# Kernel optimization log

Measured on AMD Instinct MI355X. Metric: run time of the kernel, lower is better.

The kernel has to match this reference:

```python
import jax, jax.numpy as jnp
import numpy as np

D_MODEL = 64


def _wn_weight(v, g):
    # weight_norm on Conv2d with default dim=0: per-output-channel normalization.
    # v: [O, I] (1x1 kernel squeezed), g: [O]
    norm = jnp.sqrt(jnp.sum(v * v, axis=1, keepdims=True))  # [O,1]
    return (g[:, None] / norm) * v  # [O, I]


def _conv1x1(x, v, g, b):
    # x: [B, I, L, V] -> [B, O, L, V]
    w = _wn_weight(v, g)
    return jnp.einsum('oi,bilv->bolv', w, x) + b[None, :, None, None]


def setup_inputs() -> dict:
    key = jax.random.key(0)
    ks = jax.random.split(key, 13)
    B, D, L, V = 2, D_MODEL, 4096, 4
    inp = {'queries': jax.random.normal(ks[0], (B, D, L, V), dtype=jnp.float32)}
    names = ['q', 'k', 'v', 'o']
    for i, n in enumerate(names):
        inp[n + '_v'] = jax.random.normal(ks[1 + 3 * i], (D, D), dtype=jnp.float32) * (1.0 / np.sqrt(D))
        inp[n + '_g'] = jnp.ones((D,), dtype=jnp.float32)
        inp[n + '_b'] = jnp.zeros((D,), dtype=jnp.float32)
    return inp


def reference(queries, q_v, q_g, q_b, k_v, k_g, k_b, v_v, v_g, v_b, o_v, o_g, o_b):
    B, D, L, V = queries.shape
    # 1x1 weight-normed conv projections, then permute(0,2,3,1) -> [B, L, V, D]
    q = jnp.transpose(_conv1x1(queries, q_v, q_g, q_b), (0, 2, 3, 1))
    k = jnp.transpose(_conv1x1(queries, k_v, k_g, k_b), (0, 2, 3, 1))
    v = jnp.transpose(_conv1x1(queries, v_v, v_g, v_b), (0, 2, 3, 1))
    scale = 1.0 / np.sqrt(D).astype(np.float32)
    # scores: [B, V(heads), L, S]
    scores = jnp.einsum('blhe,bshe->bhls', q, k)
    A = jax.nn.softmax(scale * scores, axis=-1)  # dropout p=0 -> identity
    out = jnp.einsum('bhls,bshd->blhd', A, v)  # [B, L, V, D]
    out = jnp.transpose(out, (0, 3, 1, 2))  # [B, D, L, V]
    out = _conv1x1(out, o_v, o_g, o_b)
    return queries + out
```

## Files before the change

### kernel.cpp

```cpp
#include <hip/hip_runtime.h>
#include <math.h>

#define D 64
#define L 4096
#define H 4
#define B 2
#define NBH 8
#define SPLIT 4
#define KTILES (L/64/SPLIT)
#define QSCALE 0.18033688011112042f

typedef unsigned short ushort_t;
typedef __attribute__((ext_vector_type(8)))  __bf16 bf16x8;
typedef __attribute__((ext_vector_type(2)))  __bf16 bf16x2;
typedef __attribute__((ext_vector_type(16))) float  f32x16;

union U4 { unsigned u[4]; bf16x8 v; };

#if __has_builtin(__builtin_amdgcn_exp2f)
__device__ __forceinline__ float EXP2(float x){ return __builtin_amdgcn_exp2f(x); }
#else
__device__ __forceinline__ float EXP2(float x){
    float r; asm("v_exp_f32 %0, %1" : "=v"(r) : "v"(x)); return r;
}
#endif

__device__ __forceinline__ unsigned pk(float lo, float hi){
    bf16x2 t; t.x = (__bf16)lo; t.y = (__bf16)hi;
    return __builtin_bit_cast(unsigned, t);
}
__device__ __forceinline__ ushort_t f2bf(float x){
    __bf16 h = (__bf16)x; return __builtin_bit_cast(ushort_t, h);
}
__device__ __forceinline__ float bf2f(ushort_t u){
    unsigned x = ((unsigned)u) << 16; return __builtin_bit_cast(float, x);
}

__device__ __forceinline__ void gload16(const void* g, void* l){
    __builtin_amdgcn_global_load_lds(
        (const __attribute__((address_space(1))) unsigned*)g,
        (__attribute__((address_space(3))) unsigned*)l, 16, 0, 0);
}

__device__ __forceinline__ bf16x8 ldfrag(const ushort_t* buf, int row, int cb){
    return *(const bf16x8*)(buf + row*64 + ((cb ^ (row&7)) << 3));
}

__global__ void wn_kernel(const float* __restrict__ qv, const float* __restrict__ qg,
                          const float* __restrict__ kv, const float* __restrict__ kg,
                          const float* __restrict__ vv, const float* __restrict__ vg,
                          const float* __restrict__ ov, const float* __restrict__ og,
                          float* __restrict__ W)
{
    int m = blockIdx.x;
    const float* v = (m==0)?qv:(m==1)?kv:(m==2)?vv:ov;
    const float* g = (m==0)?qg:(m==1)?kg:(m==2)?vg:og;
    int o = threadIdx.x;
    float ss = 0.f;
    #pragma unroll 8
    for (int i=0;i<D;i++){ float x = v[o*D+i]; ss += x*x; }
    float sc = g[o] / sqrtf(ss);
    #pragma unroll 8
    for (int i=0;i<D;i++) W[m*D*D + o*D + i] = sc * v[o*D+i];
}

__global__ __launch_bounds__(256) void proj_qkv_kernel(
    const float* __restrict__ X, const float* __restrict__ W,
    const float* __restrict__ qb, const float* __restrict__ kb, const float* __restrict__ vb,
    unsigned* __restrict__ Qd, unsigned* __restrict__ Kd, unsigned* __restrict__ Vtd)
{
    int chunk = blockIdx.x, b = blockIdx.y, m = blockIdx.z;
    const float* bias = (m==0)?qb:(m==1)?kb:vb;
    const float* Wm = W + m*(D*D);

    __shared__ __align__(16) float Xs[64][68];
    __shared__ __align__(16) float Wb[64][68];
    __shared__ __align__(16) float Os[64][68];

    int t = threadIdx.x;
    int p0 = chunk*64;
    const float* Xb = X + (size_t)b*D*(L*H);
    for (int idx=t; idx<1024; idx+=256){
        int o = idx>>4, i4 = idx&15;
        *(float4*)&Wb[o][i4*4] = *(const float4*)&Wm[o*64 + i4*4];
    }
    for (int idx=t; idx<1024; idx+=256){
        int i = idx>>4, p4 = idx&15;
        *(float4*)&Xs[i][p4*4] = *(const float4*)&Xb[(size_t)i*(L*H) + p0 + p4*4];
    }
    __syncthreads();

    int pg = t&15, og = t>>4;
    float acc[4][4];
    #pragma unroll
    for (int pp=0;pp<4;pp++)
        #pragma unroll
        for (int oo=0;oo<4;oo++) acc[pp][oo]=0.f;

    #pragma unroll 4
    for (int i4=0;i4<16;i4++){
        float4 xr[4], wr[4];
        #pragma unroll
        for (int di=0;di<4;di++) xr[di] = *(const float4*)&Xs[i4*4+di][pg*4];
        #pragma unroll
        for (int oo=0;oo<4;oo++) wr[oo] = *(const float4*)&Wb[og*4+oo][i4*4];
        #pragma unroll
        for (int pp=0;pp<4;pp++){
            #pragma unroll
            for (int oo=0;oo<4;oo++){
                acc[pp][oo] += ((const float*)&xr[0])[pp]*wr[oo].x
                             + ((const float*)&xr[1])[pp]*wr[oo].y
                             + ((const float*)&xr[2])[pp]*wr[oo].z
                             + ((const float*)&xr[3])[pp]*wr[oo].w;
            }
        }
    }
    float b4[4];
    #pragma unroll
    for (int oo=0;oo<4;oo++) b4[oo] = bias[og*4+oo];
    #pragma unroll
    for (int pp=0;pp<4;pp++){
        float4 o4 = make_float4(acc[pp][0]+b4[0], acc[pp][1]+b4[1],
                                acc[pp][2]+b4[2], acc[pp][3]+b4[3]);
        *(float4*)&Os[pg*4+pp][og*4] = o4;
    }
    __syncthreads();

    if (m == 2){
        #pragma unroll
        for (int g=0; g<4; ++g){
            for (int idx=t; idx<512; idx+=256){
                int d = idx>>3, li = idx&7;
                unsigned val = pk(Os[8*li + g][d], Os[8*li + 4 + g][d]);
                Vtd[((unsigned)(b*H+g)*D + d)*(L/2) + chunk*8 + li] = val;
            }
        }
    } else {
        unsigned* dst = (m==0)?Qd:Kd;
        float sc = (m==0)? QSCALE : 1.0f;
        for (int idx=t; idx<2048; idx+=256){
            int r = idx>>5, o2 = idx&31;
            int p = p0+r, l=p>>2, v=p&3;
            unsigned base = (((unsigned)(b*H+v)*L + l)*D + 2*o2) >> 1;
            dst[base] = pk(Os[r][2*o2]*sc, Os[r][2*o2+1]*sc);
        }
    }
}

__global__ __launch_bounds__(256) void attn_kernel(
    const ushort_t* __restrict__ Qg, const ushort_t* __restrict__ Kg,
    const ushort_t* __restrict__ VTg, ushort_t* __restrict__ OTp,
    float* __restrict__ Lsum)
{
    __shared__ __align__(16) ushort_t KB[2][4096];
    __shared__ __align__(16) ushort_t VB[2][4096];

    int t = threadIdx.x;
    int lane = t & 63;
    int wv = t >> 6;
    int l31 = lane & 31;
    int hi  = lane >> 5;
    int bh  = blockIdx.y;
    int sp  = blockIdx.z;
    int q0  = blockIdx.x*128 + wv*32;
    int kbase = sp*KTILES;

    const ushort_t* Qbh = Qg  + (size_t)bh*L*D;
    const ushort_t* Kbh = Kg  + (size_t)bh*L*D;
    const ushort_t* Vbh = VTg + (size_t)bh*D*L;

    bf16x8 qf[4];
    {
        const ushort_t* qr = Qbh + (size_t)(q0 + l31)*D + hi*8;
        qf[0] = *(const bf16x8*)(qr);
        qf[1] = *(const bf16x8*)(qr + 16);
        qf[2] = *(const bf16x8*)(qr + 32);
        qf[3] = *(const bf16x8*)(qr + 48);
    }

    int srow = lane>>3;
    int scb  = (lane&7) ^ (srow&7);

    auto stage = [&](int kt, int bi){
        const ushort_t* Ks = Kbh + (size_t)kt*(64*D);
        #pragma unroll
        for (int c=0;c<2;c++){
            int chunk = wv*2+c;
            gload16(Ks + (chunk*8+srow)*64 + scb*8, &KB[bi][chunk*512]);
        }
        #pragma unroll
        for (int c=0;c<2;c++){
            int chunk = wv*2+c;
            gload16(Vbh + (size_t)(chunk*8+srow)*L + kt*64 + scb*8, &VB[bi][chunk*512]);
        }
    };

    f32x16 o0, o1;
    #pragma unroll
    for (int r=0;r<16;r++){ o0[r]=0.f; o1[r]=0.f; }
    float lrun = 0.f;

    stage(kbase, 0);
    __syncthreads();
    int cur = 0;

    for (int nt=0; nt<KTILES; nt++){
        if (nt < KTILES-1) stage(kbase+nt+1, cur^1);

        f32x16 s0, s1;
        #pragma unroll
        for (int r=0;r<16;r++){ s0[r]=0.f; s1[r]=0.f; }
        __builtin_amdgcn_s_setprio(1);
        #pragma unroll
        for (int st=0; st<4; st++){
            bf16x8 a0 = ldfrag(KB[cur], l31,    st*2+hi);
            bf16x8 a1 = ldfrag(KB[cur], 32+l31, st*2+hi);
            s0 = __builtin_amdgcn_mfma_f32_32x32x16_bf16(a0, qf[st], s0, 0,0,0);
            s1 = __builtin_amdgcn_mfma_f32_32x32x16_bf16(a1, qf[st], s1, 0,0,0);
        }
        __builtin_amdgcn_s_setprio(0);

        float pa=0.f, pb=0.f, pc=0.f, pd=0.f;
        #pragma unroll
        for (int r=0;r<16;r+=4){
            s0[r]   = EXP2(s0[r]);   pa += s0[r];
            s0[r+1] = EXP2(s0[r+1]); pb += s0[r+1];
            s0[r+2] = EXP2(s0[r+2]); pc += s0[r+2];
            s0[r+3] = EXP2(s0[r+3]); pd += s0[r+3];
            s1[r]   = EXP2(s1[r]);   pa += s1[r];
            s1[r+1] = EXP2(s1[r+1]); pb += s1[r+1];
            s1[r+2] = EXP2(s1[r+2]); pc += s1[r+2];
            s1[r+3] = EXP2(s1[r+3]); pd += s1[r+3];
        }
        float psum = (pa+pb)+(pc+pd);
        psum += __shfl_xor(psum, 32);
        lrun += psum;

        bf16x8 pf[4];
        #pragma unroll
        for (int ks=0; ks<4; ks++){
            const int b8 = (ks&1)*8;
            #define EV(j) ((ks<2) ? s0[b8+(j)] : s1[b8+(j)])
            unsigned a  = pk(EV(0), EV(1));
            unsigned b2 = pk(EV(2), EV(3));
            unsigned c2 = pk(EV(4), EV(5));
            unsigned d2 = pk(EV(6), EV(7));
            #undef EV
            unsigned s1x = __shfl_xor(hi ? a  : c2, 32);
            unsigned s2x = __shfl_xor(hi ? b2 : d2, 32);
            U4 u;
            u.u[0] = hi ? s1x : a;
            u.u[1] = hi ? s2x : b2;
            u.u[2] = hi ? c2  : s1x;
            u.u[3] = hi ? d2  : s2x;
            pf[ks] = u.v;
        }

        __builtin_amdgcn_s_setprio(1);
        #pragma unroll
        for (int ks=0; ks<4; ks++){
            bf16x8 a0 = ldfrag(VB[cur], l31,    ks*2+hi);
            bf16x8 a1 = ldfrag(VB[cur], 32+l31, ks*2+hi);
            o0 = __builtin_amdgcn_mfma_f32_32x32x16_bf16(a0, pf[ks], o0, 0,0,0);
            o1 = __builtin_amdgcn_mfma_f32_32x32x16_bf16(a1, pf[ks], o1, 0,0,0);
        }
        __builtin_amdgcn_s_setprio(0);

        __syncthreads();
        cur ^= 1;
    }

    ushort_t* Ob = OTp + (size_t)(sp*NBH+bh)*D*L + q0 + l31;
    #pragma unroll
    for (int r=0;r<16;r++){
        int d = (r&3) + 8*(r>>2) + 4*hi;
        Ob[(size_t)d*L]      = f2bf(o0[r]);
        Ob[(size_t)(d+32)*L] = f2bf(o1[r]);
    }
    if (hi == 0)
        Lsum[(size_t)(sp*NBH+bh)*L + q0 + l31] = lrun;
}

__global__ __launch_bounds__(256) void proj_out_kernel(
    const ushort_t* __restrict__ OTp, const float* __restrict__ Lsum,
    const float* __restrict__ W, const float* __restrict__ ob,
    const float* __restrict__ queries, float* __restrict__ out)
{
    int chunk = blockIdx.x, b = blockIdx.y;
    __shared__ __align__(16) float Xs[64][68];
    __shared__ __align__(16) float Wb[64][68];
    __shared__ __align__(16) float Os[64][68];
    __shared__ float F[64];
    int t = threadIdx.x;
    const float* Wm = W + 3*(D*D);
    int p0 = chunk*64;

    for (int idx=t; idx<1024; idx+=256){
        int d = idx>>4, i4 = idx&15;
        *(float4*)&Wb[d][i4*4] = *(const float4*)&Wm[d*64 + i4*4];
    }
    if (t < 64){
        int p = p0+t, l = p>>2, v = p&3, bh = b*H+v;
        float dn = 0.f;
        #pragma unroll
        for (int s=0;s<SPLIT;s++) dn += Lsum[(size_t)(s*NBH+bh)*L + l];
        F[t] = 1.0f/dn;
    }
    __syncthreads();

    for (int idx=t; idx<4096; idx+=256){
        int v = idx>>10, i = (idx>>4)&63, pg = idx&15;
        int p = pg*4+v, bh = b*H+v;
        size_t g0 = ((size_t)bh*D + i)*L + (p0>>2) + pg;
        float a = 0.f;
        #pragma unroll
        for (int s=0;s<SPLIT;s++)
            a += bf2f(OTp[(size_t)(s*NBH)*D*L + g0]);
        Xs[i][p] = a * F[p];
    }
    __syncthreads();

    int pg = t&15, og = t>>4;
    float acc[4][4];
    #pragma unroll
    for (int pp=0;pp<4;pp++)
        #pragma unroll
        for (int dd=0;dd<4;dd++) acc[pp][dd]=0.f;

    #pragma unroll 4
    for (int i4=0;i4<16;i4++){
        float4 xr[4], wr[4];
        #pragma unroll
        for (int di=0;di<4;di++) xr[di] = *(const float4*)&Xs[i4*4+di][pg*4];
        #pragma unroll
        for (int dd=0;dd<4;dd++) wr[dd] = *(const float4*)&Wb[og*4+dd][i4*4];
        #pragma unroll
        for (int pp=0;pp<4;pp++){
            #pragma unroll
            for (int dd=0;dd<4;dd++){
                acc[pp][dd] += ((const float*)&xr[0])[pp]*wr[dd].x
                             + ((const float*)&xr[1])[pp]*wr[dd].y
                             + ((const float*)&xr[2])[pp]*wr[dd].z
                             + ((const float*)&xr[3])[pp]*wr[dd].w;
            }
        }
    }
    float b4[4];
    #pragma unroll
    for (int dd=0;dd<4;dd++) b4[dd] = ob[og*4+dd];
    #pragma unroll
    for (int dd=0;dd<4;dd++){
        float4 o4 = make_float4(acc[0][dd]+b4[dd], acc[1][dd]+b4[dd],
                                acc[2][dd]+b4[dd], acc[3][dd]+b4[dd]);
        *(float4*)&Os[og*4+dd][pg*4] = o4;
    }
    __syncthreads();

    const float* Qr = queries + (size_t)b*(D*L*H) + p0;
    float* Or = out + (size_t)b*(D*L*H) + p0;
    for (int idx=t; idx<1024; idx+=256){
        int d = idx>>4, p4 = idx&15;
        float4 q4 = *(const float4*)&Qr[(size_t)d*(L*H) + p4*4];
        float4 s4 = *(const float4*)&Os[d][p4*4];
        float4 r4 = make_float4(q4.x+s4.x, q4.y+s4.y, q4.z+s4.z, q4.w+s4.w);
        *(float4*)&Or[(size_t)d*(L*H) + p4*4] = r4;
    }
}

extern "C" void kernel_launch(void* const* d_in, const int* in_sizes, int n_in,
                              void* d_out, int out_size, void* d_ws, size_t ws_size,
                              hipStream_t stream)
{
    const float* queries = (const float*)d_in[0];
    const float* qv=(const float*)d_in[1], *qg=(const float*)d_in[2], *qb=(const float*)d_in[3];
    const float* kv=(const float*)d_in[4], *kg=(const float*)d_in[5], *kb=(const float*)d_in[6];
    const float* vv=(const float*)d_in[7], *vg=(const float*)d_in[8], *vb=(const float*)d_in[9];
    const float* ov=(const float*)d_in[10], *og=(const float*)d_in[11], *obias=(const float*)d_in[12];

    char* ws = (char*)d_ws;
    float*    Wbuf = (float*)ws;
    unsigned* Qb   = (unsigned*)(ws + (1<<16));
    unsigned* Kb2  = (unsigned*)(ws + (1<<16) + (1<<22));
    unsigned* VTb  = (unsigned*)(ws + (1<<16) + 2*(1<<22));
    ushort_t* OTp  = (ushort_t*)(ws + (1<<16) + 3*(1<<22));
    float*    Lsum = (float*)   (ws + (1<<16) + 3*(1<<22) + (1<<24));

    wn_kernel<<<4, 64, 0, stream>>>(qv,qg,kv,kg,vv,vg,ov,og,Wbuf);
    proj_qkv_kernel<<<dim3(256,2,3), 256, 0, stream>>>(queries, Wbuf, qb,kb,vb, Qb,Kb2,VTb);
    attn_kernel<<<dim3(32,NBH,SPLIT), 256, 0, stream>>>((const ushort_t*)Qb,
        (const ushort_t*)Kb2, (const ushort_t*)VTb, OTp, Lsum);
    proj_out_kernel<<<dim3(256,2), 256, 0, stream>>>(OTp, Lsum, Wbuf, obias, queries, (float*)d_out);
}
```

Before: 176.0 us.

## Shrink attention blocks to 2 waves and store partial outputs row-major via LDS

The attention kernel now launches 128-thread blocks (two waves, 64 queries) over twice as many blocks, and each wave stages more K/V chunks. Partial outputs are first repacked through LDS into an [L, D] bf16 layout and written with coalesced 16-byte stores, replacing the scattered 2-byte transposed stores. The output projection reads that new layout as 32-bit pairs. The aim is more blocks for occupancy and cheaper global writes, at the cost of more K/V staging per query, since each block reloads the full key range for fewer queries.

Result: slower. 187.6 us (+6.6%).

```diff
diff --git a/kernel.cpp b/kernel.cpp
--- a/kernel.cpp
+++ b/kernel.cpp
@@ -17,20 +17,13 @@
 
 union U4 { unsigned u[4]; bf16x8 v; };
 
-#if __has_builtin(__builtin_amdgcn_exp2f)
-__device__ __forceinline__ float EXP2(float x){ return __builtin_amdgcn_exp2f(x); }
-#else
 __device__ __forceinline__ float EXP2(float x){
     float r; asm("v_exp_f32 %0, %1" : "=v"(r) : "v"(x)); return r;
 }
-#endif
 
 __device__ __forceinline__ unsigned pk(float lo, float hi){
     bf16x2 t; t.x = (__bf16)lo; t.y = (__bf16)hi;
     return __builtin_bit_cast(unsigned, t);
-}
-__device__ __forceinline__ ushort_t f2bf(float x){
-    __bf16 h = (__bf16)x; return __builtin_bit_cast(ushort_t, h);
 }
 __device__ __forceinline__ float bf2f(ushort_t u){
     unsigned x = ((unsigned)u) << 16; return __builtin_bit_cast(float, x);
@@ -147,7 +140,7 @@
     }
 }
 
-__global__ __launch_bounds__(256) void attn_kernel(
+__global__ __launch_bounds__(128) void attn_kernel(
     const ushort_t* __restrict__ Qg, const ushort_t* __restrict__ Kg,
     const ushort_t* __restrict__ VTg, ushort_t* __restrict__ OTp,
     float* __restrict__ Lsum)
@@ -162,7 +155,7 @@
     int hi  = lane >> 5;
     int bh  = blockIdx.y;
     int sp  = blockIdx.z;
-    int q0  = blockIdx.x*128 + wv*32;
+    int q0  = blockIdx.x*64 + wv*32;
     int kbase = sp*KTILES;
 
     const ushort_t* Qbh = Qg  + (size_t)bh*L*D;
@@ -184,13 +177,13 @@
     auto stage = [&](int kt, int bi){
         const ushort_t* Ks = Kbh + (size_t)kt*(64*D);
         #pragma unroll
-        for (int c=0;c<2;c++){
-            int chunk = wv*2+c;
+        for (int c=0;c<4;c++){
+            int chunk = wv*4+c;
             gload16(Ks + (chunk*8+srow)*64 + scb*8, &KB[bi][chunk*512]);
         }
         #pragma unroll
-        for (int c=0;c<2;c++){
-            int chunk = wv*2+c;
+        for (int c=0;c<4;c++){
+            int chunk = wv*4+c;
             gload16(Vbh + (size_t)(chunk*8+srow)*L + kt*64 + scb*8, &VB[bi][chunk*512]);
         }
     };
@@ -270,12 +263,27 @@
         cur ^= 1;
     }
 
-    ushort_t* Ob = OTp + (size_t)(sp*NBH+bh)*D*L + q0 + l31;
-    #pragma unroll
-    for (int r=0;r<16;r++){
-        int d = (r&3) + 8*(r>>2) + 4*hi;
-        Ob[(size_t)d*L]      = f2bf(o0[r]);
-        Ob[(size_t)(d+32)*L] = f2bf(o1[r]);
+    {
+        unsigned* KB32 = (unsigned*)KB;
+        int row = wv*32 + l31;
+        int msk = (row&7)<<2;
+        #pragma unroll
+        for (int j=0;j<8;j++){
+            int r = 2*j;
+            int c0 = ((r&3)>>1) + 4*(r>>2) + 2*hi;
+            KB32[row*32 + ((c0     ) ^ msk)] = pk(o0[r], o0[r+1]);
+            KB32[row*32 + ((c0 + 16) ^ msk)] = pk(o1[r], o1[r+1]);
+        }
+        __syncthreads();
+        unsigned* OTp32 = (unsigned*)OTp;
+        size_t gbase = ((size_t)(sp*NBH+bh)*L + (size_t)blockIdx.x*64) * 32;
+        #pragma unroll
+        for (int j=0;j<4;j++){
+            int id = t + j*128;
+            int rr = id>>3, k = id&7;
+            uint4 vv2 = *(const uint4*)&KB32[rr*32 + ((k*4) ^ ((rr&7)<<2))];
+            *(uint4*)&OTp32[gbase + (size_t)id*4] = vv2;
+        }
     }
     if (hi == 0)
         Lsum[(size_t)(sp*NBH+bh)*L + q0 + l31] = lrun;
@@ -308,15 +316,23 @@
     }
     __syncthreads();
 
-    for (int idx=t; idx<4096; idx+=256){
-        int v = idx>>10, i = (idx>>4)&63, pg = idx&15;
-        int p = pg*4+v, bh = b*H+v;
-        size_t g0 = ((size_t)bh*D + i)*L + (p0>>2) + pg;
-        float a = 0.f;
-        #pragma unroll
-        for (int s=0;s<SPLIT;s++)
-            a += bf2f(OTp[(size_t)(s*NBH)*D*L + g0]);
-        Xs[i][p] = a * F[p];
+    const unsigned* OTp32 = (const unsigned*)OTp;
+    for (int rnd=0; rnd<8; rnd++){
+        int id = t + rnd*256;
+        int c = id&31, lloc = (id>>5)&15, v = id>>9;
+        int bh = b*H+v;
+        size_t lglob = (size_t)(p0>>2) + lloc;
+        float a0 = 0.f, a1 = 0.f;
+        #pragma unroll
+        for (int s=0;s<SPLIT;s++){
+            unsigned u = OTp32[((size_t)(s*NBH+bh)*L + lglob)*32 + c];
+            a0 += bf2f((ushort_t)(u & 0xffffu));
+            a1 += bf2f((ushort_t)(u >> 16));
+        }
+        int pos = lloc*4 + v;
+        float f = F[pos];
+        Xs[2*c][pos]   = a0*f;
+        Xs[2*c+1][pos] = a1*f;
     }
     __syncthreads();
 
@@ -387,7 +403,7 @@
 
     wn_kernel<<<4, 64, 0, stream>>>(qv,qg,kv,kg,vv,vg,ov,og,Wbuf);
     proj_qkv_kernel<<<dim3(256,2,3), 256, 0, stream>>>(queries, Wbuf, qb,kb,vb, Qb,Kb2,VTb);
-    attn_kernel<<<dim3(32,NBH,SPLIT), 256, 0, stream>>>((const ushort_t*)Qb,
+    attn_kernel<<<dim3(64,NBH,SPLIT), 128, 0, stream>>>((const ushort_t*)Qb,
         (const ushort_t*)Kb2, (const ushort_t*)VTb, OTp, Lsum);
     proj_out_kernel<<<dim3(256,2), 256, 0, stream>>>(OTp, Lsum, Wbuf, obias, queries, (float*)d_out);
 }
```
